# Kernel tuning notes

Measured on AMD Instinct MI355X. Metric: run time of the kernel, lower is better.

## Reference

```python
import jax, jax.numpy as jnp
import numpy as np
from functools import partial

SAMPLE_RATE = 44100
CUTOFF_HZ = 20.0
# one-pole high-pass coefficient: y[i] = x[i] - x[i-1] + alpha * y[i-1]
ALPHA = float(np.exp(-2.0 * np.pi * CUTOFF_HZ / SAMPLE_RATE))


def setup_inputs() -> dict:
    key = jax.random.key(0)
    k1, k2, k3, k4 = jax.random.split(key, 4)
    B, N = 64, 262144
    return {
        "x": jax.random.normal(k1, (B, N), dtype=jnp.float32),
        "drive": jax.random.uniform(k2, (B, 1), dtype=jnp.float32),
        "bias": jax.random.uniform(k3, (B, 1), dtype=jnp.float32),
        "mix": jax.random.uniform(k4, (B, 1), dtype=jnp.float32),
        "type_idx": 0,
    }


def _waveshape(processed, type_idx):
    if type_idx == 0:
        return jnp.tanh(processed)
    elif type_idx == 1:
        return jnp.clip(processed, -1.0, 1.0)
    elif type_idx == 2:
        return jnp.abs(jnp.remainder(processed + 1.0, 4.0) - 2.0) - 1.0
    elif type_idx == 3:
        return jnp.sin(processed * (np.pi / 2))
    else:
        return processed / (1.0 + jnp.abs(processed))


def _high_pass_filter(x):
    # x: [B, N]; sequential first-order IIR over the time axis via lax.scan
    B = x.shape[0]
    zeros = jnp.zeros((B,), dtype=x.dtype)

    def step(carry, xt):
        last_x, last_y = carry
        yt = xt - last_x + ALPHA * last_y
        return (xt, yt), yt

    _, yT = jax.lax.scan(step, (zeros, zeros), x.T)  # yT: [N, B]
    return yT.T


def reference(x, drive, bias, mix, type_idx):
    drive_gain = jnp.power(10.0, drive * 2.4)
    dc_offset = bias * 2.0 - 1.0
    processed = (x + dc_offset) * drive_gain
    distorted = _waveshape(processed, type_idx)
    distorted = _high_pass_filter(distorted)
    return (1.0 - mix) * x + mix * distorted
```

## Files before the change

kernel.cpp:

```cpp
#include <hip/hip_runtime.h>
#include <math.h>

#define TPB 512
#define WAVES (TPB / 64)
#define PER_WAVE 512
#define CHUNK (WAVES * PER_WAVE)
#define NB 16
#define HALO 2048

typedef float v4f __attribute__((ext_vector_type(4)));

template<int CTRL, int RM, int BM, bool BC>
__device__ __forceinline__ float dppf(float v) {
    return __int_as_float(__builtin_amdgcn_update_dpp(
        0, __float_as_int(v), CTRL, RM, BM, BC));
}

__device__ __forceinline__ float readlane_f(float v, int l) {
    return __int_as_float(__builtin_amdgcn_readlane(__float_as_int(v), l));
}

__device__ __forceinline__ void stage16(const float* __restrict__ g, float* l) {
    __builtin_amdgcn_global_load_lds(
        (const __attribute__((address_space(1))) unsigned int*)g,
        (__attribute__((address_space(3))) unsigned int*)l, 16, 0, 0);
}

__device__ __forceinline__ float scan_iir(float v, float mo1, float mo2,
                                          float mo4, float mo8,
                                          float w1, float w2) {
    float b;
    b = dppf<0x111, 0xF, 0xF, true >(v); v = fmaf(mo1, b, v);
    b = dppf<0x112, 0xF, 0xF, true >(v); v = fmaf(mo2, b, v);
    b = dppf<0x114, 0xF, 0xF, true >(v); v = fmaf(mo4, b, v);
    b = dppf<0x118, 0xF, 0xF, true >(v); v = fmaf(mo8, b, v);
    b = dppf<0x142, 0xA, 0xF, false>(v); v = fmaf(w1,  b, v);
    b = dppf<0x143, 0xC, 0xF, false>(v); v = fmaf(w2,  b, v);
    return v;
}

__device__ __forceinline__ float shape(float xs, int ty, float g, float dc,
                                       float c1, float c0) {
    if (ty == 0) {
        float e2 = __builtin_amdgcn_exp2f(fmaf(xs, c1, c0));
        return fmaf(-2.0f, __builtin_amdgcn_rcpf(e2 + 1.0f), 1.0f);
    }
    float p = (xs + dc) * g;
    if (ty == 1) {
        return fminf(fmaxf(p, -1.0f), 1.0f);
    } else if (ty == 2) {
        float r = p + 1.0f;
        float rem = r - 4.0f * floorf(r * 0.25f);
        return fabsf(rem - 2.0f) - 1.0f;
    } else if (ty == 3) {
        return __sinf(p * 1.5707963267948966f);
    } else {
        return p / (1.0f + fabsf(p));
    }
}

__global__ void __launch_bounds__(TPB, 6)
dist_kernel(const float* __restrict__ x,
            const float* __restrict__ drive,
            const float* __restrict__ bias,
            const float* __restrict__ mix,
            const int* __restrict__ type_idx,
            float* __restrict__ out,
            int N, float alpha, float beta)
{
    const int row  = blockIdx.y;
    const int bx   = blockIdx.x;
    const int tid  = threadIdx.x;
    const int lane = tid & 63;
    const int wv   = tid >> 6;
    const int ty   = *type_idx;

    const int nChunks = (N + CHUNK - 1) / CHUNK;
    const int cpb = (nChunks + NB - 1) / NB;
    const int cFirst = bx * cpb;
    if (cFirst >= nChunks) return;
    const int cLast = min(cFirst + cpb, nChunks);
    const int spanStart = cFirst * CHUNK;

    const long long rowBase = (long long)row * (long long)N;
    const float* __restrict__ xr = x + rowBase;
    float* __restrict__ outr = out + rowBase;

    __shared__ float sbuf[2][CHUNK];
    __shared__ float wtot[2][WAVES];

    const int ldsBase = wv * PER_WAVE;
    const int wvOff   = ldsBase + lane * 4;

    if (spanStart + CHUNK <= N) {
        stage16(xr + spanStart + ldsBase + lane * 4,       &sbuf[0][ldsBase]);
        stage16(xr + spanStart + ldsBase + 256 + lane * 4, &sbuf[0][ldsBase + 256]);
    } else {
        #pragma unroll
        for (int h = 0; h < 2; ++h) {
            const int idx = ldsBase + h * 256 + lane * 4;
            const int j = spanStart + idx;
            v4f v;
            v.x = (j + 0 < N) ? xr[j + 0] : 0.0f;
            v.y = (j + 1 < N) ? xr[j + 1] : 0.0f;
            v.z = (j + 2 < N) ? xr[j + 2] : 0.0f;
            v.w = (j + 3 < N) ? xr[j + 3] : 0.0f;
            *reinterpret_cast<v4f*>(&sbuf[0][idx]) = v;
        }
    }

    const float g  = exp2f(drive[row] * 7.972672880099267f);
    const float dc = bias[row] * 2.0f - 1.0f;
    const float mm = mix[row];
    const float om = 1.0f - mm;
    const float c1 = g * 2.8853900817779268f;
    const float c0 = dc * c1;

    const float A2 = alpha * alpha;
    const float A4 = A2 * A2;
    const float A8 = A4 * A4;
    const float A16 = A8 * A8;
    const float A32 = A16 * A16;
    const float A64 = A32 * A32;
    const float A128 = A64 * A64;
    const float A256 = A128 * A128;
    const float A512 = A256 * A256;

    float p15 = 1.0f;
    {
        float b = A4; const int n = lane & 15;
        #pragma unroll
        for (int i = 0; i < 4; ++i) { if ((n >> i) & 1) p15 *= b; b *= b; }
    }
    const float p31 = (lane & 16) ? p15 * A64  : p15;
    const float apl = (lane & 32) ? p31 * A128 : p31;
    const float w1 = A4 * p15;
    const float w2 = A4 * p31;

    float carry = 0.0f;
    if (bx > 0) {
        const int j = spanStart - HALO + wv * 256 + lane * 4;
        const v4f hx = *reinterpret_cast<const v4f*>(xr + j);
        float r = shape(hx.x, ty, g, dc, c1, c0);
        r = fmaf(alpha, r, shape(hx.y, ty, g, dc, c1, c0));
        r = fmaf(alpha, r, shape(hx.z, ty, g, dc, c1, c0));
        r = fmaf(alpha, r, shape(hx.w, ty, g, dc, c1, c0));
        const float s = scan_iir(r, A4, A8, A16, A32, w1, w2);
        if (lane == 63) wtot[1][wv] = s;
    }
    __syncthreads();
    if (bx > 0) {
        #pragma unroll
        for (int w = 0; w < WAVES; ++w) carry = fmaf(A256, carry, wtot[1][w]);
    }

    int par = 0;
    for (int c = cFirst; c < cLast; ++c, par ^= 1) {
        const int cb = c * CHUNK;

        float iv[2];
        #pragma unroll
        for (int k = 0; k < 2; ++k) {
            const v4f xv = *reinterpret_cast<const v4f*>(&sbuf[par][wvOff + k * 256]);
            float acc = shape(xv.x, ty, g, dc, c1, c0);
            acc = fmaf(alpha, acc, shape(xv.y, ty, g, dc, c1, c0));
            acc = fmaf(alpha, acc, shape(xv.z, ty, g, dc, c1, c0));
            acc = fmaf(alpha, acc, shape(xv.w, ty, g, dc, c1, c0));
            iv[k] = scan_iir(acc, A4, A8, A16, A32, w1, w2);
        }
        const float Tk0 = readlane_f(iv[0], 63);
        const float Tk1 = readlane_f(iv[1], 63);
        if (lane == 0) wtot[par][wv] = fmaf(A256, Tk0, Tk1);
        __syncthreads();

        float P = carry;
        for (int w = 0; w < wv; ++w) P = fmaf(A512, P, wtot[par][w]);
        #pragma unroll
        for (int w = 0; w < WAVES; ++w) carry = fmaf(A512, carry, wtot[par][w]);

        if (c + 1 < cLast) {
            const int nb = cb + CHUNK;
            if (nb + CHUNK <= N) {
                stage16(xr + nb + ldsBase + lane * 4,       &sbuf[par ^ 1][ldsBase]);
                stage16(xr + nb + ldsBase + 256 + lane * 4, &sbuf[par ^ 1][ldsBase + 256]);
            } else {
                #pragma unroll
                for (int h = 0; h < 2; ++h) {
                    const int idx = ldsBase + h * 256 + lane * 4;
                    const int j = nb + idx;
                    v4f v;
                    v.x = (j + 0 < N) ? xr[j + 0] : 0.0f;
                    v.y = (j + 1 < N) ? xr[j + 1] : 0.0f;
                    v.z = (j + 2 < N) ? xr[j + 2] : 0.0f;
                    v.w = (j + 3 < N) ? xr[j + 3] : 0.0f;
                    *reinterpret_cast<v4f*>(&sbuf[par ^ 1][idx]) = v;
                }
            }
        }

        float S = 0.0f, aK = 1.0f;
        #pragma unroll
        for (int k = 0; k < 2; ++k) {
            const int j = cb + wvOff + k * 256;
            const v4f xv = *reinterpret_cast<const v4f*>(&sbuf[par][wvOff + k * 256]);
            const float d0 = shape(xv.x, ty, g, dc, c1, c0);
            const float d1 = shape(xv.y, ty, g, dc, c1, c0);
            const float d2 = shape(xv.z, ty, g, dc, c1, c0);
            const float d3 = shape(xv.w, ty, g, dc, c1, c0);
            const float Ck = fmaf(aK, P, S);
            const float ex = dppf<0x138, 0xF, 0xF, true>(iv[k]);
            float z = fmaf(apl, Ck, ex);
            v4f ov; float y;
            y = fmaf(-beta, z, d0); ov.x = fmaf(mm, y, om * xv.x); z = fmaf(alpha, z, d0);
            y = fmaf(-beta, z, d1); ov.y = fmaf(mm, y, om * xv.y); z = fmaf(alpha, z, d1);
            y = fmaf(-beta, z, d2); ov.z = fmaf(mm, y, om * xv.z); z = fmaf(alpha, z, d2);
            y = fmaf(-beta, z, d3); ov.w = fmaf(mm, y, om * xv.w);
            if (j + 4 <= N) {
                __builtin_nontemporal_store(ov, reinterpret_cast<v4f*>(outr + j));
            } else {
                if (j + 0 < N) outr[j + 0] = ov.x;
                if (j + 1 < N) outr[j + 1] = ov.y;
                if (j + 2 < N) outr[j + 2] = ov.z;
                if (j + 3 < N) outr[j + 3] = ov.w;
            }
            S = fmaf(A256, S, Tk0);
            aK *= A256;
        }
        __syncthreads();
    }
}

extern "C" void kernel_launch(void* const* d_in, const int* in_sizes, int n_in,
                              void* d_out, int out_size, void* d_ws, size_t ws_size,
                              hipStream_t stream) {
    const float* x     = (const float*)d_in[0];
    const float* drive = (const float*)d_in[1];
    const float* bias  = (const float*)d_in[2];
    const float* mixp  = (const float*)d_in[3];
    const int*   tyi   = (const int*)d_in[4];
    float* out = (float*)d_out;

    const int B = in_sizes[1];
    const int N = in_sizes[0] / B;

    const double alpha_d = exp(-2.0 * M_PI * 20.0 / 44100.0);
    const float alpha = (float)alpha_d;
    const float beta  = (float)(1.0 - alpha_d);

    dim3 grid(NB, B);
    dist_kernel<<<grid, TPB, 0, stream>>>(x, drive, bias, mixp, tyi, out, N, alpha, beta);
}
```

Before: 117.8 us.

## Process one fixed 8K span per block with halo staged in LDS

```diff
diff --git a/kernel.cpp b/kernel.cpp
--- a/kernel.cpp
+++ b/kernel.cpp
@@ -3,10 +3,10 @@
 
 #define TPB 512
 #define WAVES (TPB / 64)
-#define PER_WAVE 512
-#define CHUNK (WAVES * PER_WAVE)
-#define NB 16
+#define SPAN 8192
 #define HALO 2048
+#define TOT (SPAN + HALO)
+#define WSPAN (SPAN / WAVES)
 
 typedef float v4f __attribute__((ext_vector_type(4)));
 
@@ -75,37 +75,38 @@
     const int wv   = tid >> 6;
     const int ty   = *type_idx;
 
-    const int nChunks = (N + CHUNK - 1) / CHUNK;
-    const int cpb = (nChunks + NB - 1) / NB;
-    const int cFirst = bx * cpb;
-    if (cFirst >= nChunks) return;
-    const int cLast = min(cFirst + cpb, nChunks);
-    const int spanStart = cFirst * CHUNK;
+    const int spanStart = bx * SPAN;
 
     const long long rowBase = (long long)row * (long long)N;
     const float* __restrict__ xr = x + rowBase;
     float* __restrict__ outr = out + rowBase;
 
-    __shared__ float sbuf[2][CHUNK];
-    __shared__ float wtot[2][WAVES];
-
-    const int ldsBase = wv * PER_WAVE;
-    const int wvOff   = ldsBase + lane * 4;
-
-    if (spanStart + CHUNK <= N) {
-        stage16(xr + spanStart + ldsBase + lane * 4,       &sbuf[0][ldsBase]);
-        stage16(xr + spanStart + ldsBase + 256 + lane * 4, &sbuf[0][ldsBase + 256]);
+    __shared__ float sbuf[TOT];
+
+    const bool fullSpan = (spanStart + SPAN <= N);
+    if (fullSpan) {
+        if (bx > 0) {
+            const int gb = spanStart - HALO + wv * (TOT / WAVES);
+            const int lb = wv * (TOT / WAVES);
+            #pragma unroll
+            for (int i = 0; i < (TOT / WAVES) / 256; ++i)
+                stage16(xr + gb + i * 256 + lane * 4, &sbuf[lb + i * 256]);
+        } else {
+            const int gb = spanStart + wv * WSPAN;
+            const int lb = HALO + wv * WSPAN;
+            #pragma unroll
+            for (int i = 0; i < WSPAN / 256; ++i)
+                stage16(xr + gb + i * 256 + lane * 4, &sbuf[lb + i * 256]);
+        }
     } else {
-        #pragma unroll
-        for (int h = 0; h < 2; ++h) {
-            const int idx = ldsBase + h * 256 + lane * 4;
-            const int j = spanStart + idx;
+        for (int p = tid * 4; p < TOT; p += TPB * 4) {
+            const int j = spanStart - HALO + p;
             v4f v;
-            v.x = (j + 0 < N) ? xr[j + 0] : 0.0f;
-            v.y = (j + 1 < N) ? xr[j + 1] : 0.0f;
-            v.z = (j + 2 < N) ? xr[j + 2] : 0.0f;
-            v.w = (j + 3 < N) ? xr[j + 3] : 0.0f;
-            *reinterpret_cast<v4f*>(&sbuf[0][idx]) = v;
+            v.x = (j + 0 >= 0 && j + 0 < N) ? xr[j + 0] : 0.0f;
+            v.y = (j + 1 >= 0 && j + 1 < N) ? xr[j + 1] : 0.0f;
+            v.z = (j + 2 >= 0 && j + 2 < N) ? xr[j + 2] : 0.0f;
+            v.w = (j + 3 >= 0 && j + 3 < N) ? xr[j + 3] : 0.0f;
+            *reinterpret_cast<v4f*>(&sbuf[p]) = v;
         }
     }
 
@@ -125,6 +126,7 @@
     const float A128 = A64 * A64;
     const float A256 = A128 * A128;
     const float A512 = A256 * A256;
+    const float A1024 = A512 * A512;
 
     float p15 = 1.0f;
     {
@@ -137,96 +139,72 @@
     const float w1 = A4 * p15;
     const float w2 = A4 * p31;
 
-    float carry = 0.0f;
+    __syncthreads();
+
     if (bx > 0) {
-        const int j = spanStart - HALO + wv * 256 + lane * 4;
-        const v4f hx = *reinterpret_cast<const v4f*>(xr + j);
+        const v4f hx = *reinterpret_cast<const v4f*>(&sbuf[wv * 256 + lane * 4]);
         float r = shape(hx.x, ty, g, dc, c1, c0);
         r = fmaf(alpha, r, shape(hx.y, ty, g, dc, c1, c0));
         r = fmaf(alpha, r, shape(hx.z, ty, g, dc, c1, c0));
         r = fmaf(alpha, r, shape(hx.w, ty, g, dc, c1, c0));
         const float s = scan_iir(r, A4, A8, A16, A32, w1, w2);
-        if (lane == 63) wtot[1][wv] = s;
-    }
+        if (lane == 63) sbuf[wv * 256] = s;
+    }
+
+    float iv[4], Tk[4];
+    #pragma unroll
+    for (int k = 0; k < 4; ++k) {
+        const v4f xv = *reinterpret_cast<const v4f*>(
+            &sbuf[HALO + wv * WSPAN + k * 256 + lane * 4]);
+        float acc = shape(xv.x, ty, g, dc, c1, c0);
+        acc = fmaf(alpha, acc, shape(xv.y, ty, g, dc, c1, c0));
+        acc = fmaf(alpha, acc, shape(xv.z, ty, g, dc, c1, c0));
+        acc = fmaf(alpha, acc, shape(xv.w, ty, g, dc, c1, c0));
+        iv[k] = scan_iir(acc, A4, A8, A16, A32, w1, w2);
+        Tk[k] = readlane_f(iv[k], 63);
+    }
+    const float Tw =
+        fmaf(A256, fmaf(A256, fmaf(A256, Tk[0], Tk[1]), Tk[2]), Tk[3]);
+    if (lane == 0) sbuf[wv * 256 + 1] = Tw;
     __syncthreads();
+
+    float carry = 0.0f;
     if (bx > 0) {
         #pragma unroll
-        for (int w = 0; w < WAVES; ++w) carry = fmaf(A256, carry, wtot[1][w]);
-    }
-
-    int par = 0;
-    for (int c = cFirst; c < cLast; ++c, par ^= 1) {
-        const int cb = c * CHUNK;
-
-        float iv[2];
-        #pragma unroll
-        for (int k = 0; k < 2; ++k) {
-            const v4f xv = *reinterpret_cast<const v4f*>(&sbuf[par][wvOff + k * 256]);
-            float acc = shape(xv.x, ty, g, dc, c1, c0);
-            acc = fmaf(alpha, acc, shape(xv.y, ty, g, dc, c1, c0));
-            acc = fmaf(alpha, acc, shape(xv.z, ty, g, dc, c1, c0));
-            acc = fmaf(alpha, acc, shape(xv.w, ty, g, dc, c1, c0));
-            iv[k] = scan_iir(acc, A4, A8, A16, A32, w1, w2);
+        for (int w = 0; w < WAVES; ++w)
+            carry = fmaf(A256, carry, sbuf[w * 256]);
+    }
+    float P = carry;
+    for (int w = 0; w < wv; ++w) P = fmaf(A1024, P, sbuf[w * 256 + 1]);
+
+    float S = 0.0f, aK = 1.0f;
+    #pragma unroll
+    for (int k = 0; k < 4; ++k) {
+        const int j = spanStart + wv * WSPAN + k * 256 + lane * 4;
+        const v4f xv = *reinterpret_cast<const v4f*>(
+            &sbuf[HALO + wv * WSPAN + k * 256 + lane * 4]);
+        const float d0 = shape(xv.x, ty, g, dc, c1, c0);
+        const float d1 = shape(xv.y, ty, g, dc, c1, c0);
+        const float d2 = shape(xv.z, ty, g, dc, c1, c0);
+        const float d3 = shape(xv.w, ty, g, dc, c1, c0);
+        const float Ck = fmaf(aK, P, S);
+        const float ex = dppf<0x138, 0xF, 0xF, true>(iv[k]);
+        float z = fmaf(apl, Ck, ex);
+        v4f ov; float y;
+        y = fmaf(-beta, z, d0); ov.x = fmaf(mm, y, om * xv.x); z = fmaf(alpha, z, d0);
+        y = fmaf(-beta, z, d1); ov.y = fmaf(mm, y, om * xv.y); z = fmaf(alpha, z, d1);
+        y = fmaf(-beta, z, d2); ov.z = fmaf(mm, y, om * xv.z); z = fmaf(alpha, z, d2);
+        y = fmaf(-beta, z, d3); ov.w = fmaf(mm, y, om * xv.w);
+        if (j + 4 <= N) {
+            __builtin_nontemporal_store(ov, reinterpret_cast<v4f*>(outr + j));
+        } else {
+            if (j + 0 < N) outr[j + 0] = ov.x;
+            if (j + 1 < N) outr[j + 1] = ov.y;
+            if (j + 2 < N) outr[j + 2] = ov.z;
+            if (j + 3 < N) outr[j + 3] = ov.w;
         }
-        const float Tk0 = readlane_f(iv[0], 63);
-        const float Tk1 = readlane_f(iv[1], 63);
-        if (lane == 0) wtot[par][wv] = fmaf(A256, Tk0, Tk1);
-        __syncthreads();
-
-        float P = carry;
-        for (int w = 0; w < wv; ++w) P = fmaf(A512, P, wtot[par][w]);
-        #pragma unroll
-        for (int w = 0; w < WAVES; ++w) carry = fmaf(A512, carry, wtot[par][w]);
-
-        if (c + 1 < cLast) {
-            const int nb = cb + CHUNK;
-            if (nb + CHUNK <= N) {
-                stage16(xr + nb + ldsBase + lane * 4,       &sbuf[par ^ 1][ldsBase]);
-                stage16(xr + nb + ldsBase + 256 + lane * 4, &sbuf[par ^ 1][ldsBase + 256]);
-            } else {
-                #pragma unroll
-                for (int h = 0; h < 2; ++h) {
-                    const int idx = ldsBase + h * 256 + lane * 4;
-                    const int j = nb + idx;
-                    v4f v;
-                    v.x = (j + 0 < N) ? xr[j + 0] : 0.0f;
-                    v.y = (j + 1 < N) ? xr[j + 1] : 0.0f;
-                    v.z = (j + 2 < N) ? xr[j + 2] : 0.0f;
-                    v.w = (j + 3 < N) ? xr[j + 3] : 0.0f;
-                    *reinterpret_cast<v4f*>(&sbuf[par ^ 1][idx]) = v;
-                }
-            }
-        }
-
-        float S = 0.0f, aK = 1.0f;
-        #pragma unroll
-        for (int k = 0; k < 2; ++k) {
-            const int j = cb + wvOff + k * 256;
-            const v4f xv = *reinterpret_cast<const v4f*>(&sbuf[par][wvOff + k * 256]);
-            const float d0 = shape(xv.x, ty, g, dc, c1, c0);
-            const float d1 = shape(xv.y, ty, g, dc, c1, c0);
-            const float d2 = shape(xv.z, ty, g, dc, c1, c0);
-            const float d3 = shape(xv.w, ty, g, dc, c1, c0);
-            const float Ck = fmaf(aK, P, S);
-            const float ex = dppf<0x138, 0xF, 0xF, true>(iv[k]);
-            float z = fmaf(apl, Ck, ex);
-            v4f ov; float y;
-            y = fmaf(-beta, z, d0); ov.x = fmaf(mm, y, om * xv.x); z = fmaf(alpha, z, d0);
-            y = fmaf(-beta, z, d1); ov.y = fmaf(mm, y, om * xv.y); z = fmaf(alpha, z, d1);
-            y = fmaf(-beta, z, d2); ov.z = fmaf(mm, y, om * xv.z); z = fmaf(alpha, z, d2);
-            y = fmaf(-beta, z, d3); ov.w = fmaf(mm, y, om * xv.w);
-            if (j + 4 <= N) {
-                __builtin_nontemporal_store(ov, reinterpret_cast<v4f*>(outr + j));
-            } else {
-                if (j + 0 < N) outr[j + 0] = ov.x;
-                if (j + 1 < N) outr[j + 1] = ov.y;
-                if (j + 2 < N) outr[j + 2] = ov.z;
-                if (j + 3 < N) outr[j + 3] = ov.w;
-            }
-            S = fmaf(A256, S, Tk0);
-            aK *= A256;
-        }
-        __syncthreads();
+        S = fmaf(A256, S, Tk[k]);
+        aK *= A256;
     }
 }
 
@@ -247,6 +225,7 @@
     const float alpha = (float)alpha_d;
     const float beta  = (float)(1.0 - alpha_d);
 
-    dim3 grid(NB, B);
+    const int nSpans = (N + SPAN - 1) / SPAN;
+    dim3 grid(nSpans, B);
     dist_kernel<<<grid, TPB, 0, stream>>>(x, drive, bias, mixp, tyi, out, N, alpha, beta);
 }
```

New measurement: 116.3 us. About the same (-1.2%).

## Drop per-chunk block barrier, use manual waitcnts, and lengthen per-block spans

Applied to the files above, without the earlier changes.

```diff
diff --git a/kernel.cpp b/kernel.cpp
--- a/kernel.cpp
+++ b/kernel.cpp
@@ -2,10 +2,10 @@
 #include <math.h>
 
 #define TPB 512
-#define WAVES (TPB / 64)
+#define WAVES 8
 #define PER_WAVE 512
-#define CHUNK (WAVES * PER_WAVE)
-#define NB 16
+#define CHUNK 4096
+#define CPB 8
 #define HALO 2048
 
 typedef float v4f __attribute__((ext_vector_type(4)));
@@ -59,7 +59,7 @@
     }
 }
 
-__global__ void __launch_bounds__(TPB, 6)
+__global__ void __launch_bounds__(TPB, 4)
 dist_kernel(const float* __restrict__ x,
             const float* __restrict__ drive,
             const float* __restrict__ bias,
@@ -76,10 +76,9 @@
     const int ty   = *type_idx;
 
     const int nChunks = (N + CHUNK - 1) / CHUNK;
-    const int cpb = (nChunks + NB - 1) / NB;
-    const int cFirst = bx * cpb;
+    const int cFirst = bx * CPB;
     if (cFirst >= nChunks) return;
-    const int cLast = min(cFirst + cpb, nChunks);
+    const int cLast = min(cFirst + CPB, nChunks);
     const int spanStart = cFirst * CHUNK;
 
     const long long rowBase = (long long)row * (long long)N;
@@ -88,17 +87,24 @@
 
     __shared__ float sbuf[2][CHUNK];
     __shared__ float wtot[2][WAVES];
-
-    const int ldsBase = wv * PER_WAVE;
-    const int wvOff   = ldsBase + lane * 4;
-
+    __shared__ float htot[WAVES];
+
+    const int wb = wv * PER_WAVE;
+    const int lo = wb + lane * 4;
+
+    v4f hx;
+    const bool haveHalo = (bx > 0);
+    if (haveHalo) {
+        const int j = spanStart - HALO + wv * 256 + lane * 4;
+        hx = *reinterpret_cast<const v4f*>(xr + j);
+    }
     if (spanStart + CHUNK <= N) {
-        stage16(xr + spanStart + ldsBase + lane * 4,       &sbuf[0][ldsBase]);
-        stage16(xr + spanStart + ldsBase + 256 + lane * 4, &sbuf[0][ldsBase + 256]);
+        stage16(xr + spanStart + lo,       &sbuf[0][wb]);
+        stage16(xr + spanStart + lo + 256, &sbuf[0][wb + 256]);
     } else {
         #pragma unroll
         for (int h = 0; h < 2; ++h) {
-            const int idx = ldsBase + h * 256 + lane * 4;
+            const int idx = lo + h * 256;
             const int j = spanStart + idx;
             v4f v;
             v.x = (j + 0 < N) ? xr[j + 0] : 0.0f;
@@ -138,55 +144,58 @@
     const float w2 = A4 * p31;
 
     float carry = 0.0f;
-    if (bx > 0) {
-        const int j = spanStart - HALO + wv * 256 + lane * 4;
-        const v4f hx = *reinterpret_cast<const v4f*>(xr + j);
+    if (haveHalo) {
         float r = shape(hx.x, ty, g, dc, c1, c0);
         r = fmaf(alpha, r, shape(hx.y, ty, g, dc, c1, c0));
         r = fmaf(alpha, r, shape(hx.z, ty, g, dc, c1, c0));
         r = fmaf(alpha, r, shape(hx.w, ty, g, dc, c1, c0));
         const float s = scan_iir(r, A4, A8, A16, A32, w1, w2);
-        if (lane == 63) wtot[1][wv] = s;
-    }
-    __syncthreads();
-    if (bx > 0) {
-        #pragma unroll
-        for (int w = 0; w < WAVES; ++w) carry = fmaf(A256, carry, wtot[1][w]);
-    }
+        if (lane == 63) htot[wv] = s;
+        asm volatile("s_waitcnt lgkmcnt(0)" ::: "memory");
+        __builtin_amdgcn_s_barrier();
+        __builtin_amdgcn_sched_barrier(0);
+        const v4f h0 = *reinterpret_cast<const v4f*>(&htot[0]);
+        const v4f h1 = *reinterpret_cast<const v4f*>(&htot[4]);
+        carry = h0.x;
+        carry = fmaf(A256, carry, h0.y);
+        carry = fmaf(A256, carry, h0.z);
+        carry = fmaf(A256, carry, h0.w);
+        carry = fmaf(A256, carry, h1.x);
+        carry = fmaf(A256, carry, h1.y);
+        carry = fmaf(A256, carry, h1.z);
+        carry = fmaf(A256, carry, h1.w);
+    }
+
+    asm volatile("s_waitcnt vmcnt(0)" ::: "memory");
+    __builtin_amdgcn_sched_barrier(0);
 
     int par = 0;
     for (int c = cFirst; c < cLast; ++c, par ^= 1) {
-        const int cb = c * CHUNK;
-
-        float iv[2];
+        asm volatile("s_waitcnt vmcnt(2)" ::: "memory");
+        __builtin_amdgcn_sched_barrier(0);
+
+        float iv[2], Tk[2];
         #pragma unroll
         for (int k = 0; k < 2; ++k) {
-            const v4f xv = *reinterpret_cast<const v4f*>(&sbuf[par][wvOff + k * 256]);
+            const v4f xv = *reinterpret_cast<const v4f*>(&sbuf[par][lo + k * 256]);
             float acc = shape(xv.x, ty, g, dc, c1, c0);
             acc = fmaf(alpha, acc, shape(xv.y, ty, g, dc, c1, c0));
             acc = fmaf(alpha, acc, shape(xv.z, ty, g, dc, c1, c0));
             acc = fmaf(alpha, acc, shape(xv.w, ty, g, dc, c1, c0));
             iv[k] = scan_iir(acc, A4, A8, A16, A32, w1, w2);
-        }
-        const float Tk0 = readlane_f(iv[0], 63);
-        const float Tk1 = readlane_f(iv[1], 63);
-        if (lane == 0) wtot[par][wv] = fmaf(A256, Tk0, Tk1);
-        __syncthreads();
-
-        float P = carry;
-        for (int w = 0; w < wv; ++w) P = fmaf(A512, P, wtot[par][w]);
-        #pragma unroll
-        for (int w = 0; w < WAVES; ++w) carry = fmaf(A512, carry, wtot[par][w]);
+            Tk[k] = readlane_f(iv[k], 63);
+        }
+        if (lane == 0) wtot[par][wv] = fmaf(A256, Tk[0], Tk[1]);
 
         if (c + 1 < cLast) {
-            const int nb = cb + CHUNK;
+            const int nb = (c + 1) * CHUNK;
             if (nb + CHUNK <= N) {
-                stage16(xr + nb + ldsBase + lane * 4,       &sbuf[par ^ 1][ldsBase]);
-                stage16(xr + nb + ldsBase + 256 + lane * 4, &sbuf[par ^ 1][ldsBase + 256]);
+                stage16(xr + nb + lo,       &sbuf[par ^ 1][wb]);
+                stage16(xr + nb + lo + 256, &sbuf[par ^ 1][wb + 256]);
             } else {
                 #pragma unroll
                 for (int h = 0; h < 2; ++h) {
-                    const int idx = ldsBase + h * 256 + lane * 4;
+                    const int idx = lo + h * 256;
                     const int j = nb + idx;
                     v4f v;
                     v.x = (j + 0 < N) ? xr[j + 0] : 0.0f;
@@ -198,16 +207,30 @@
             }
         }
 
-        float S = 0.0f, aK = 1.0f;
+        asm volatile("s_waitcnt lgkmcnt(0)" ::: "memory");
+        __builtin_amdgcn_s_barrier();
+        __builtin_amdgcn_sched_barrier(0);
+
+        const v4f t0 = *reinterpret_cast<const v4f*>(&wtot[par][0]);
+        const v4f t1 = *reinterpret_cast<const v4f*>(&wtot[par][4]);
+        const float ww[8] = {t0.x, t0.y, t0.z, t0.w, t1.x, t1.y, t1.z, t1.w};
+        float P = carry;
+        #pragma unroll
+        for (int w = 0; w < 7; ++w)
+            if (w < wv) P = fmaf(A512, P, ww[w]);
+        #pragma unroll
+        for (int w = 0; w < 8; ++w)
+            carry = fmaf(A512, carry, ww[w]);
+
         #pragma unroll
         for (int k = 0; k < 2; ++k) {
-            const int j = cb + wvOff + k * 256;
-            const v4f xv = *reinterpret_cast<const v4f*>(&sbuf[par][wvOff + k * 256]);
+            const int j = c * CHUNK + lo + k * 256;
+            const v4f xv = *reinterpret_cast<const v4f*>(&sbuf[par][lo + k * 256]);
             const float d0 = shape(xv.x, ty, g, dc, c1, c0);
             const float d1 = shape(xv.y, ty, g, dc, c1, c0);
             const float d2 = shape(xv.z, ty, g, dc, c1, c0);
             const float d3 = shape(xv.w, ty, g, dc, c1, c0);
-            const float Ck = fmaf(aK, P, S);
+            const float Ck = (k == 0) ? P : fmaf(A256, P, Tk[0]);
             const float ex = dppf<0x138, 0xF, 0xF, true>(iv[k]);
             float z = fmaf(apl, Ck, ex);
             v4f ov; float y;
@@ -223,10 +246,7 @@
                 if (j + 2 < N) outr[j + 2] = ov.z;
                 if (j + 3 < N) outr[j + 3] = ov.w;
             }
-            S = fmaf(A256, S, Tk0);
-            aK *= A256;
-        }
-        __syncthreads();
+        }
     }
 }
 
@@ -247,6 +267,8 @@
     const float alpha = (float)alpha_d;
     const float beta  = (float)(1.0 - alpha_d);
 
-    dim3 grid(NB, B);
+    const int nChunks = (N + CHUNK - 1) / CHUNK;
+    const int nSpans = (nChunks + CPB - 1) / CPB;
+    dim3 grid(nSpans, B);
     dist_kernel<<<grid, TPB, 0, stream>>>(x, drive, bias, mixp, tyi, out, N, alpha, beta);
 }
```

New measurement: 118.7 us. Within noise of the previous version (+0.8%).
